# Kernel tuning notes

Hardware: AMD Instinct MI355X
Metric: run time of the kernel (lower is better)

The kernel has to match this reference:

```python
import jax, jax.numpy as jnp
import numpy as np
from jax import lax

STRIDE = (1, 1, 1, 1)
PADDING = (1, 1, 1, 1)
DILATION = (1, 1, 1, 1)


def setup_inputs() -> dict:
    key = jax.random.key(0)
    k1, k2, k3 = jax.random.split(key, 3)
    x = jax.random.normal(k1, (4, 32, 8, 24, 24, 24), dtype=jnp.float32)
    # weight layout matches torch ConvTranspose: (C_in, C_out, l_k, d_k, h_k, w_k)
    weight = jax.random.normal(k2, (32, 32, 3, 3, 3, 3), dtype=jnp.float32) * 0.05
    bias = jax.random.normal(k3, (32,), dtype=jnp.float32) * 0.05
    return {"x": x, "weight": weight, "bias": bias}


def _conv_transpose_4d(x, weight):
    # Transposed conv == conv with lhs dilated by stride, kernel spatially
    # flipped, and padding d*(k-1) - p on each side of each spatial dim.
    # Output size per dim: (i-1)*s - 2p + d*(k-1) + 1, identical to the
    # torch module's looped ConvTranspose3d + temporal scatter-add.
    ksp = weight.shape[2:]
    pads = [(d * (k - 1) - p, d * (k - 1) - p)
            for k, p, d in zip(ksp, PADDING, DILATION)]
    w = jnp.flip(weight, axis=(2, 3, 4, 5))  # (C_in, C_out, l, d, h, w)
    return lax.conv_general_dilated(
        x, w,
        window_strides=(1, 1, 1, 1),
        padding=pads,
        lhs_dilation=STRIDE,
        rhs_dilation=DILATION,
        dimension_numbers=("NCLDHW", "IOLDHW", "NCLDHW"),
    )


def reference(x, weight, bias):
    out = _conv_transpose_4d(x, weight)
    return out + bias.reshape(1, -1, 1, 1, 1, 1)
```

## Files before the change

kernel.cpp:

```cpp
#include <hip/hip_runtime.h>

#define NN 4
#define CC 32
#define LL 8
#define DD 24
#define HH 24
#define WW 24

typedef short  bf16x8  __attribute__((ext_vector_type(8)));
typedef float  f32x16  __attribute__((ext_vector_type(16)));
typedef unsigned short ushort8 __attribute__((ext_vector_type(8)));

#define XP_CHUNKS (4 * 4 * 8 * 26 * 26 * 26)
#define XP_ELEMS  (XP_CHUNKS * 8)
#define AG_ELEMS  (4 * 3 * 3 * 5 * 64 * 8)

__device__ __forceinline__ unsigned short f2bf(float f) {
    union { float f; unsigned u; } v; v.f = f;
    unsigned r = v.u + 0x7FFFu + ((v.u >> 16) & 1u);
    return (unsigned short)(r >> 16);
}

__device__ __forceinline__ void gload16(const void* g, void* l) {
    __builtin_amdgcn_global_load_lds(
        (const __attribute__((address_space(1))) unsigned int*)g,
        (__attribute__((address_space(3))) unsigned int*)l, 16, 0, 0);
}

__global__ __launch_bounds__(256) void prep_x(const float* __restrict__ x,
                                              unsigned short* __restrict__ xp) {
    const int c  = blockIdx.x * 256 + threadIdx.x;
    const int wp = c % 26;
    const int t1 = c / 26;
    const int hp = t1 % 26;
    const int t2 = t1 / 26;
    const int dp = t2 % 26;
    const int t3 = t2 / 26;
    const int l  = t3 & 7;
    const int t4 = t3 >> 3;
    const int n  = t4 & 3;
    const int cig = t4 >> 2;
    const int dx = dp - 1, hx = hp - 1, wx = wp - 1;
    ushort8 v = {0, 0, 0, 0, 0, 0, 0, 0};
    if ((unsigned)dx < DD && (unsigned)hx < HH && (unsigned)wx < WW) {
        const float* src = x + (((((size_t)n * CC + cig * 8) * LL + l) * DD + dx) * HH + hx) * WW + wx;
#pragma unroll
        for (int ci = 0; ci < 8; ++ci)
            v[ci] = f2bf(src[(size_t)ci * (LL * DD * HH * WW)]);
    }
    *reinterpret_cast<ushort8*>(xp + (size_t)c * 8) = v;
}

__global__ __launch_bounds__(256) void prep_w(const float* __restrict__ wgt,
                                              unsigned short* __restrict__ Ag) {
    const int i  = blockIdx.x * 256 + threadIdx.x;
    const int j  = i & 7;
    const int ln = (i >> 3) & 63;
    const int s  = (i >> 9) % 5;
    const int r  = (i >> 9) / 5;
    const int qd = r % 3;
    const int ql = (r / 3) % 3;
    const int cig = r / 9;
    const int co = ln & 31, gg = ln >> 5;
    const int tl = 2 * s + gg;
    unsigned short v = 0;
    if (tl <= 8) {
        const int tap = ql * 27 + qd * 9 + tl;
        v = f2bf(wgt[(size_t)((cig * 8 + j) * CC + co) * 81 + 80 - tap]);
    }
    Ag[i] = v;
}

__global__ __launch_bounds__(384, 4) void convt4d_main(
    const unsigned short* __restrict__ xp, const unsigned short* __restrict__ Ag,
    const float* __restrict__ bias, float* __restrict__ out)
{
    __shared__ __align__(16) unsigned short xs[2][676 * 8];
    __shared__ __align__(16) unsigned short As[2][320 * 8];

    int bid = (int)blockIdx.x;
    bid = (bid & 7) * 96 + (bid >> 3);
    const int n = bid / (LL * DD);
    const int l = (bid / DD) % LL;
    const int d = bid % DD;

    const int t    = (int)threadIdx.x;
    const int lane = t & 63;
    const int wave = t >> 6;
    const int g    = lane >> 5;
    const int dh   = (lane >> 3) & 3;
    const int dw   = lane & 7;
    const int h0   = wave * 4;

    const int ql0 = (l == 0) ? 1 : 0;
    const int nql = 3 - (l == 0) - (l == 7);
    const int nst = 4 * nql * 3;

    f32x16 acc[3];
#pragma unroll
    for (int i = 0; i < 3; ++i)
#pragma unroll
        for (int j = 0; j < 16; ++j) acc[i][j] = 0.f;

    const int base0 = ((h0 + dh) * 26 + dw) * 16;

    auto issue = [&](int id, int buf) {
        const int qd  = id % 3;
        const int r   = id / 3;
        const int ql  = ql0 + r % nql;
        const int cig = r / nql;
        const int lx  = l + ql - 1;
        const unsigned short* xsrc =
            xp + (size_t)((((cig * 4 + n) * 8 + lx) * 26) + (d + qd)) * (676 * 8);
        gload16(xsrc + (size_t)t * 8, (char*)xs[buf] + (size_t)t * 16);
        if (t + 384 < 676)
            gload16(xsrc + (size_t)(t + 384) * 8, (char*)xs[buf] + (size_t)(t + 384) * 16);
        const unsigned short* asrc = Ag + (size_t)((cig * 3 + ql) * 3 + qd) * 2560;
        if (t < 320)
            gload16(asrc + (size_t)t * 8, (char*)As[buf] + (size_t)t * 16);
    };

    issue(0, 0);

#pragma unroll 1
    for (int st = 0; st < nst; ++st) {
        const int buf = st & 1;
        __syncthreads();
        if (st + 1 < nst) issue(st + 1, buf ^ 1);

        const char* xsb = (const char*)xs[buf];
#pragma unroll
        for (int s = 0; s < 5; ++s) {
            bf16x8 a = *reinterpret_cast<const bf16x8*>(&As[buf][(s * 64 + lane) * 8]);
            const int t0 = 2 * s;
            const int t1 = (2 * s + 1 > 8) ? 8 : 2 * s + 1;
            const int tl = g ? t1 : t0;
            const int off = ((tl / 3) * 26 + (tl % 3)) * 16;
            const char* bp = xsb + (base0 + off);
#pragma unroll
            for (int nt = 0; nt < 3; ++nt) {
                bf16x8 b = *reinterpret_cast<const bf16x8*>(bp + nt * 128);
                acc[nt] = __builtin_amdgcn_mfma_f32_32x32x16_bf16(a, b, acc[nt], 0, 0, 0);
            }
        }
    }

#pragma unroll
    for (int r = 0; r < 16; ++r) {
        const int co = (r & 3) + 8 * (r >> 2) + 4 * g;
        const float bv = bias[co];
        size_t ob = (((((size_t)n * CC + co) * LL + l) * DD + d) * HH + (h0 + dh)) * WW + dw;
        out[ob]      = acc[0][r] + bv;
        out[ob + 8]  = acc[1][r] + bv;
        out[ob + 16] = acc[2][r] + bv;
    }
}

extern "C" void kernel_launch(void* const* d_in, const int* in_sizes, int n_in,
                              void* d_out, int out_size, void* d_ws, size_t ws_size,
                              hipStream_t stream) {
    const float* x    = (const float*)d_in[0];
    const float* wgt  = (const float*)d_in[1];
    const float* bias = (const float*)d_in[2];
    float* out = (float*)d_out;

    unsigned short* xp = (unsigned short*)d_ws;
    unsigned short* Ag = xp + XP_ELEMS;

    prep_x<<<XP_CHUNKS / 256, 256, 0, stream>>>(x, xp);
    prep_w<<<AG_ELEMS / 256, 256, 0, stream>>>(wgt, Ag);
    convt4d_main<<<NN * LL * DD, 384, 0, stream>>>(xp, Ag, bias, out);
}
```

Before: 99.14 us.

## Restructure MFMA K-split to 16 channels per tap and fuse prep kernels

Changes the K decomposition of the transposed-conv GEMM. Previously the 9 (h,w) taps were packed pairwise across half-waves with 8 channels, which padded 9 taps to 10. Now each MFMA covers one tap with 16 input channels, split across the half-waves. The x workspace is interleaved as two 8-channel groups per position, and a padded-row LDS layout (53 units per row) is introduced. Weights are no longer staged through LDS; each wave reads its 9 A fragments directly from global memory. The two prep kernels are merged into one launch, and the occupancy hint drops from 4 to 3 blocks. This removes the padding waste and half of the pipeline stages, at the cost of larger LDS tiles, more registers and uncached per-stage global weight reads.

```diff
diff --git a/kernel.cpp b/kernel.cpp
--- a/kernel.cpp
+++ b/kernel.cpp
@@ -11,9 +11,9 @@
 typedef float  f32x16  __attribute__((ext_vector_type(16)));
 typedef unsigned short ushort8 __attribute__((ext_vector_type(8)));
 
-#define XP_CHUNKS (4 * 4 * 8 * 26 * 26 * 26)
+#define XP_CHUNKS 2249728
 #define XP_ELEMS  (XP_CHUNKS * 8)
-#define AG_ELEMS  (4 * 3 * 3 * 5 * 64 * 8)
+#define AG_ELEMS  82944
 
 __device__ __forceinline__ unsigned short f2bf(float f) {
     union { float f; unsigned u; } v; v.f = f;
@@ -27,56 +27,59 @@
         (__attribute__((address_space(3))) unsigned int*)l, 16, 0, 0);
 }
 
-__global__ __launch_bounds__(256) void prep_x(const float* __restrict__ x,
-                                              unsigned short* __restrict__ xp) {
-    const int c  = blockIdx.x * 256 + threadIdx.x;
-    const int wp = c % 26;
-    const int t1 = c / 26;
-    const int hp = t1 % 26;
-    const int t2 = t1 / 26;
-    const int dp = t2 % 26;
-    const int t3 = t2 / 26;
-    const int l  = t3 & 7;
-    const int t4 = t3 >> 3;
-    const int n  = t4 & 3;
-    const int cig = t4 >> 2;
-    const int dx = dp - 1, hx = hp - 1, wx = wp - 1;
-    ushort8 v = {0, 0, 0, 0, 0, 0, 0, 0};
-    if ((unsigned)dx < DD && (unsigned)hx < HH && (unsigned)wx < WW) {
-        const float* src = x + (((((size_t)n * CC + cig * 8) * LL + l) * DD + dx) * HH + hx) * WW + wx;
+__global__ __launch_bounds__(256) void prep(const float* __restrict__ x,
+                                            const float* __restrict__ wgt,
+                                            unsigned short* __restrict__ xp,
+                                            unsigned short* __restrict__ Ag) {
+    const int id = blockIdx.x * 256 + threadIdx.x;
+    if (id < XP_CHUNKS) {
+        const int wp = id % 26;
+        const int r  = id / 26;
+        const int g  = r & 1;
+        const int r2 = r >> 1;
+        const int hp = r2 % 26;
+        const int slab = r2 / 26;
+        const int dp = slab % 26;
+        const int s2 = slab / 26;
+        const int l  = s2 & 7;
+        const int n  = (s2 >> 3) & 3;
+        const int cig = s2 >> 5;
+        const int dx = dp - 1, hx = hp - 1, wx = wp - 1;
+        ushort8 v = {0, 0, 0, 0, 0, 0, 0, 0};
+        if ((unsigned)dx < DD && (unsigned)hx < HH && (unsigned)wx < WW) {
+            const int ci0 = cig * 16 + g * 8;
+            const float* src = x + ((((size_t)n * CC + ci0) * LL + l) * DD + dx) * (HH * WW)
+                             + hx * WW + wx;
 #pragma unroll
-        for (int ci = 0; ci < 8; ++ci)
-            v[ci] = f2bf(src[(size_t)ci * (LL * DD * HH * WW)]);
+            for (int ci = 0; ci < 8; ++ci)
+                v[ci] = f2bf(src[(size_t)ci * (LL * DD * HH * WW)]);
+        }
+        const size_t dstc = ((size_t)r2 * 26 + wp) * 2 + g;
+        *reinterpret_cast<ushort8*>(xp + dstc * 8) = v;
+    } else {
+        const int i = id - XP_CHUNKS;
+        if (i < AG_ELEMS) {
+            const int j  = i & 7;
+            const int ln = (i >> 3) & 63;
+            const int rest = i >> 9;
+            const int s  = rest % 9;
+            const int r  = rest / 9;
+            const int qd = r % 3;
+            const int ql = (r / 3) % 3;
+            const int cig = r / 9;
+            const int co = ln & 31, gg = ln >> 5;
+            const int ci = cig * 16 + gg * 8 + j;
+            const int tap = ql * 27 + qd * 9 + s;
+            Ag[i] = f2bf(wgt[((size_t)ci * CC + co) * 81 + 80 - tap]);
+        }
     }
-    *reinterpret_cast<ushort8*>(xp + (size_t)c * 8) = v;
 }
 
-__global__ __launch_bounds__(256) void prep_w(const float* __restrict__ wgt,
-                                              unsigned short* __restrict__ Ag) {
-    const int i  = blockIdx.x * 256 + threadIdx.x;
-    const int j  = i & 7;
-    const int ln = (i >> 3) & 63;
-    const int s  = (i >> 9) % 5;
-    const int r  = (i >> 9) / 5;
-    const int qd = r % 3;
-    const int ql = (r / 3) % 3;
-    const int cig = r / 9;
-    const int co = ln & 31, gg = ln >> 5;
-    const int tl = 2 * s + gg;
-    unsigned short v = 0;
-    if (tl <= 8) {
-        const int tap = ql * 27 + qd * 9 + tl;
-        v = f2bf(wgt[(size_t)((cig * 8 + j) * CC + co) * 81 + 80 - tap]);
-    }
-    Ag[i] = v;
-}
-
-__global__ __launch_bounds__(384, 4) void convt4d_main(
+__global__ __launch_bounds__(384, 3) void convt4d_main(
     const unsigned short* __restrict__ xp, const unsigned short* __restrict__ Ag,
     const float* __restrict__ bias, float* __restrict__ out)
 {
-    __shared__ __align__(16) unsigned short xs[2][676 * 8];
-    __shared__ __align__(16) unsigned short As[2][320 * 8];
+    __shared__ __align__(16) unsigned short xs[2][1378 * 8];
 
     int bid = (int)blockIdx.x;
     bid = (bid & 7) * 96 + (bid >> 3);
@@ -94,7 +97,7 @@
 
     const int ql0 = (l == 0) ? 1 : 0;
     const int nql = 3 - (l == 0) - (l == 7);
-    const int nst = 4 * nql * 3;
+    const int nst = 6 * nql;
 
     f32x16 acc[3];
 #pragma unroll
@@ -102,22 +105,27 @@
 #pragma unroll
         for (int j = 0; j < 16; ++j) acc[i][j] = 0.f;
 
-    const int base0 = ((h0 + dh) * 26 + dw) * 16;
+    const int eb = ((h0 + dh) * 53 + dw * 2 + g) * 8;
 
-    auto issue = [&](int id, int buf) {
-        const int qd  = id % 3;
-        const int r   = id / 3;
+    auto issue = [&](int st, int buf) {
+        const int qd  = st % 3;
+        const int r   = st / 3;
         const int ql  = ql0 + r % nql;
         const int cig = r / nql;
         const int lx  = l + ql - 1;
-        const unsigned short* xsrc =
-            xp + (size_t)((((cig * 4 + n) * 8 + lx) * 26) + (d + qd)) * (676 * 8);
-        gload16(xsrc + (size_t)t * 8, (char*)xs[buf] + (size_t)t * 16);
-        if (t + 384 < 676)
-            gload16(xsrc + (size_t)(t + 384) * 8, (char*)xs[buf] + (size_t)(t + 384) * 16);
-        const unsigned short* asrc = Ag + (size_t)((cig * 3 + ql) * 3 + qd) * 2560;
-        if (t < 320)
-            gload16(asrc + (size_t)t * 8, (char*)As[buf] + (size_t)t * 16);
+        const unsigned short* base =
+            xp + (size_t)((((cig * 4 + n) * 8 + lx) * 26) + (d + qd)) * (676 * 16);
+        unsigned short* dst = xs[buf];
+#pragma unroll
+        for (int k = 0; k < 4; ++k) {
+            const int v = t + k * 384;
+            if (k < 3 || v < 1378) {
+                int row = v / 53;
+                int su  = v - row;
+                if (su > 1351) su = 1351;
+                gload16(base + (size_t)su * 8, (char*)dst + (size_t)v * 16);
+            }
+        }
     };
 
     issue(0, 0);
@@ -128,19 +136,26 @@
         __syncthreads();
         if (st + 1 < nst) issue(st + 1, buf ^ 1);
 
-        const char* xsb = (const char*)xs[buf];
+        const int qd  = st % 3;
+        const int r   = st / 3;
+        const int ql  = ql0 + r % nql;
+        const int cig = r / nql;
+        const unsigned short* ab =
+            Ag + (size_t)(cig * 9 + ql * 3 + qd) * 4608 + lane * 8;
+        bf16x8 A[9];
 #pragma unroll
-        for (int s = 0; s < 5; ++s) {
-            bf16x8 a = *reinterpret_cast<const bf16x8*>(&As[buf][(s * 64 + lane) * 8]);
-            const int t0 = 2 * s;
-            const int t1 = (2 * s + 1 > 8) ? 8 : 2 * s + 1;
-            const int tl = g ? t1 : t0;
-            const int off = ((tl / 3) * 26 + (tl % 3)) * 16;
-            const char* bp = xsb + (base0 + off);
+        for (int s = 0; s < 9; ++s)
+            A[s] = *reinterpret_cast<const bf16x8*>(ab + s * 512);
+
+        const unsigned short* xb = xs[buf] + eb;
+#pragma unroll
+        for (int s = 0; s < 9; ++s) {
+            const int qh = s / 3, qw = s % 3;
+            const int o = (qh * 53 + qw * 2) * 8;
 #pragma unroll
             for (int nt = 0; nt < 3; ++nt) {
-                bf16x8 b = *reinterpret_cast<const bf16x8*>(bp + nt * 128);
-                acc[nt] = __builtin_amdgcn_mfma_f32_32x32x16_bf16(a, b, acc[nt], 0, 0, 0);
+                bf16x8 b = *reinterpret_cast<const bf16x8*>(xb + o + nt * 128);
+                acc[nt] = __builtin_amdgcn_mfma_f32_32x32x16_bf16(A[s], b, acc[nt], 0, 0, 0);
             }
         }
     }
@@ -167,7 +182,6 @@
     unsigned short* xp = (unsigned short*)d_ws;
     unsigned short* Ag = xp + XP_ELEMS;
 
-    prep_x<<<XP_CHUNKS / 256, 256, 0, stream>>>(x, xp);
-    prep_w<<<AG_ELEMS / 256, 256, 0, stream>>>(wgt, Ag);
+    prep<<<(XP_CHUNKS + AG_ELEMS) / 256, 256, 0, stream>>>(x, wgt, xp, Ag);
     convt4d_main<<<NN * LL * DD, 384, 0, stream>>>(xp, Ag, bias, out);
 }
```

New measurement: 104.0 us. +4.9%, slower.
